# Kernel optimization log

Hardware: AMD Instinct MI355X
Metric: run time of the kernel (lower is better)

Reference implementation:

```python
import jax, jax.numpy as jnp
import numpy as np

B, S, D = 4, 1024, 1024
DH = D // 8  # q/k projection dim


def setup_inputs() -> dict:
    key = jax.random.key(0)
    ks = jax.random.split(key, 16)
    std = 0.02
    inp = {
        "drums": jax.random.normal(ks[0], (B, S, D), jnp.float32),
        "vocals": jax.random.normal(ks[1], (B, S, D), jnp.float32),
        "bass": jax.random.normal(ks[2], (B, S, D), jnp.float32),
        "other": jax.random.normal(ks[3], (B, S, D), jnp.float32),
        # Linear weights stored [in, out] (transposed vs torch's [out, in])
        "DqW": jax.random.normal(ks[4], (D, DH), jnp.float32) * std,
        "Dqb": jax.random.normal(ks[5], (DH,), jnp.float32) * std,
        "DkW": jax.random.normal(ks[6], (D, DH), jnp.float32) * std,
        "Dkb": jax.random.normal(ks[7], (DH,), jnp.float32) * std,
        "DvW": jax.random.normal(ks[8], (D, D), jnp.float32) * std,
        "Dvb": jax.random.normal(ks[9], (D,), jnp.float32) * std,
        "VqW": jax.random.normal(ks[10], (D, DH), jnp.float32) * std,
        "Vqb": jax.random.normal(ks[11], (DH,), jnp.float32) * std,
        "VkW": jax.random.normal(ks[12], (D, DH), jnp.float32) * std,
        "Vkb": jax.random.normal(ks[13], (DH,), jnp.float32) * std,
        "VvW": jax.random.normal(ks[14], (D, D), jnp.float32) * std,
        "Vvb": jax.random.normal(ks[15], (D,), jnp.float32) * std,
    }
    return inp


def reference(drums, vocals, bass, other,
              DqW, Dqb, DkW, Dkb, DvW, Dvb,
              VqW, Vqb, VkW, Vkb, VvW, Vvb):
    d_model = drums.shape[-1]
    lin = lambda x, W, b: jnp.einsum("bsd,de->bse", x, W) + b
    # drums uses D_* projections; vocals/bass/other all use V_* (faithful to source)
    q = jnp.concatenate([lin(drums, DqW, Dqb), lin(vocals, VqW, Vqb),
                         lin(bass, VqW, Vqb), lin(other, VqW, Vqb)], axis=-2)
    k = jnp.concatenate([lin(drums, DkW, Dkb), lin(vocals, VkW, Vkb),
                         lin(bass, VkW, Vkb), lin(other, VkW, Vkb)], axis=-2)
    v = jnp.concatenate([lin(drums, DvW, Dvb), lin(vocals, VvW, Vvb),
                         lin(bass, VvW, Vvb), lin(other, VvW, Vvb)], axis=-2)
    # scores: [B, 4S, 4S]; dropout is identity at inference
    scores = jnp.einsum("bqe,bke->bqk", q, k) / jnp.sqrt(jnp.asarray(d_model, q.dtype))
    attn = jax.nn.softmax(scores, axis=-1)
    out = jnp.einsum("bqk,bkd->bqd", attn, v)  # [B, 4S, D]
    return out.mean(axis=-2)  # [B, D]
```

## Files before the change

### kernel.cpp

```cpp
#include <hip/hip_runtime.h>
#include <hip/hip_bf16.h>

typedef __bf16 bf16x8 __attribute__((ext_vector_type(8)));
typedef float  f32x4  __attribute__((ext_vector_type(4)));

#define MFMA(a, b, c) __builtin_amdgcn_mfma_f32_16x16x32_bf16((a), (b), (c), 0, 0, 0)

static constexpr float SC_L2E = 0.03125f * 1.44269504088896341f;
static constexpr float INV_NQ = 1.0f / 4096.0f;

__device__ inline bf16x8 ld_cvt_bf8(const float* __restrict__ p) {
    f32x4 x0 = *(const f32x4*)p;
    f32x4 x1 = *(const f32x4*)(p + 4);
    bf16x8 r;
    r[0] = (__bf16)x0[0]; r[1] = (__bf16)x0[1]; r[2] = (__bf16)x0[2]; r[3] = (__bf16)x0[3];
    r[4] = (__bf16)x1[0]; r[5] = (__bf16)x1[1]; r[6] = (__bf16)x1[2]; r[7] = (__bf16)x1[3];
    return r;
}

__global__ __launch_bounds__(256) void kT(const float* __restrict__ Dq, const float* __restrict__ Vq,
                                          const float* __restrict__ Dk, const float* __restrict__ Vk,
                                          __bf16* __restrict__ Wt) {
    int idx = blockIdx.x * 256 + threadIdx.x;
    int m   = idx >> 17;
    int rem = idx & 131071;
    int r   = rem >> 7;
    int c   = rem & 127;
    const float* W = (m == 0) ? Dq : (m == 1) ? Vq : (m == 2) ? Dk : Vk;
    Wt[(size_t)m * 131072 + (size_t)c * 1024 + r] = (__bf16)W[rem];
}

__global__ __launch_bounds__(256) void kProj(
    const float* __restrict__ drums, const float* __restrict__ vocals,
    const float* __restrict__ bass,  const float* __restrict__ other,
    const float* __restrict__ Dqb, const float* __restrict__ Vqb,
    const float* __restrict__ Dkb, const float* __restrict__ Vkb,
    const __bf16* __restrict__ Wt, __bf16* __restrict__ Qb, __bf16* __restrict__ Kb) {
    int grow0 = blockIdx.x * 64;
    int b    = grow0 >> 12;
    int r4   = grow0 & 4095;
    int stem = r4 >> 10;
    int rin  = r4 & 1023;

    const float* X = (stem == 0) ? drums : (stem == 1) ? vocals : (stem == 2) ? bass : other;
    const __bf16* WQ = Wt + (size_t)((stem == 0) ? 0 : 1) * 131072;
    const __bf16* WK = Wt + (size_t)((stem == 0) ? 2 : 3) * 131072;
    const float* bQ = (stem == 0) ? Dqb : Vqb;
    const float* bK = (stem == 0) ? Dkb : Vkb;

    int lane = threadIdx.x & 63, wid = threadIdx.x >> 6;
    int l16 = lane & 15, g = lane >> 4;
    int wr = rin + wid * 16;

    f32x4 aQ[8], aK[8];
#pragma unroll
    for (int j = 0; j < 8; j++) { aQ[j] = (f32x4){0.f,0.f,0.f,0.f}; aK[j] = (f32x4){0.f,0.f,0.f,0.f}; }

    const float* xr = X + ((size_t)b * 1024 + wr + l16) * 1024;
    for (int k0 = 0; k0 < 1024; k0 += 32) {
        int ko = k0 + g * 8;
        bf16x8 a = ld_cvt_bf8(xr + ko);
#pragma unroll
        for (int cf = 0; cf < 8; cf++) {
            bf16x8 wq = *(const bf16x8*)(WQ + (size_t)(cf * 16 + l16) * 1024 + ko);
            aQ[cf] = MFMA(a, wq, aQ[cf]);
            bf16x8 wk = *(const bf16x8*)(WK + (size_t)(cf * 16 + l16) * 1024 + ko);
            aK[cf] = MFMA(a, wk, aK[cf]);
        }
    }
    size_t obase = (size_t)b * 4096 + (size_t)stem * 1024;
#pragma unroll
    for (int cf = 0; cf < 8; cf++) {
        int col = cf * 16 + l16;
        float bvq = bQ[col], bvk = bK[col];
#pragma unroll
        for (int r = 0; r < 4; r++) {
            int row = wr + g * 4 + r;
            Qb[(obase + row) * 128 + col] = (__bf16)(aQ[cf][r] + bvq);
            Kb[(obase + row) * 128 + col] = (__bf16)(aK[cf][r] + bvk);
        }
    }
}

__global__ __launch_bounds__(256) void kRowSum(const __bf16* __restrict__ Qb,
                                               const __bf16* __restrict__ Kb,
                                               float* __restrict__ lsum) {
    __shared__ uint4 ktile[1024];
    int bx = blockIdx.x;
    int cc = bx & 7, tile = (bx >> 3) & 31, b = bx >> 8;
    int lane = threadIdx.x & 63, wid = threadIdx.x >> 6;
    int l16 = lane & 15, g = lane >> 4;
    int R  = tile * 128 + wid * 32;
    int C0 = cc * 512;
    const __bf16* Qr = Qb + (size_t)b * 4096 * 128;
    const __bf16* Kr = Kb + (size_t)b * 4096 * 128;

    bf16x8 a[2][4];
#pragma unroll
    for (int rf = 0; rf < 2; rf++)
#pragma unroll
        for (int kf = 0; kf < 4; kf++)
            a[rf][kf] = *(const bf16x8*)(Qr + (size_t)(R + rf * 16 + l16) * 128 + kf * 32 + g * 8);

    int sr = threadIdx.x >> 2, sseg = threadIdx.x & 3;
    char* kbc = (char*)ktile;
    int swm = (sr & 7) << 4;

    uint4 st[4];
    {
        const char* src = (const char*)(Kr + (size_t)(C0 + sr) * 128) + sseg * 64;
#pragma unroll
        for (int j = 0; j < 4; j++) st[j] = *(const uint4*)(src + j * 16);
    }

    float rs[2][4] = {};
    for (int s = 0; s < 8; ++s) {
        __syncthreads();
#pragma unroll
        for (int j = 0; j < 4; j++)
            *(uint4*)(kbc + sr * 256 + ((sseg * 64 + j * 16) ^ swm)) = st[j];
        __syncthreads();
        if (s < 7) {
            const char* src = (const char*)(Kr + (size_t)(C0 + (s + 1) * 64 + sr) * 128) + sseg * 64;
#pragma unroll
            for (int j = 0; j < 4; j++) st[j] = *(const uint4*)(src + j * 16);
        }
#pragma unroll
        for (int ctl = 0; ctl < 4; ++ctl) {
            int r2 = ctl * 16 + l16;
            int rm = (r2 & 7) << 4;
            f32x4 acc0 = (f32x4){0.f,0.f,0.f,0.f};
            f32x4 acc1 = (f32x4){0.f,0.f,0.f,0.f};
#pragma unroll
            for (int kf = 0; kf < 4; kf++) {
                bf16x8 bv = *(const bf16x8*)(kbc + r2 * 256 + ((kf * 64 + g * 16) ^ rm));
                acc0 = MFMA(a[0][kf], bv, acc0);
                acc1 = MFMA(a[1][kf], bv, acc1);
            }
#pragma unroll
            for (int r = 0; r < 4; r++) {
                rs[0][r] += exp2f(acc0[r] * SC_L2E);
                rs[1][r] += exp2f(acc1[r] * SC_L2E);
            }
        }
    }
#pragma unroll
    for (int rf = 0; rf < 2; rf++)
#pragma unroll
        for (int r = 0; r < 4; r++) {
            float v = rs[rf][r];
#pragma unroll
            for (int m = 1; m < 16; m <<= 1) v += __shfl_xor(v, m);
            if (l16 == 0) atomicAdd(&lsum[(size_t)b * 4096 + R + rf * 16 + g * 4 + r], v);
        }
}

__global__ __launch_bounds__(256) void kInv(const float* __restrict__ lsum, float* __restrict__ linv) {
    int i = (blockIdx.x * 256 + threadIdx.x) * 4;
    f32x4 v = *(const f32x4*)(lsum + i);
    f32x4 r = (f32x4){1.f / v[0], 1.f / v[1], 1.f / v[2], 1.f / v[3]};
    *(f32x4*)(linv + i) = r;
}

__global__ __launch_bounds__(256) void kColSum(const __bf16* __restrict__ Qb,
                                               const __bf16* __restrict__ Kb,
                                               const float* __restrict__ linv,
                                               float* __restrict__ wsum) {
    __shared__ uint4 qtile[1024];
    __shared__ float li[512];
    int bx = blockIdx.x;
    int rc = bx & 7, tile = (bx >> 3) & 31, b = bx >> 8;
    int lane = threadIdx.x & 63, wid = threadIdx.x >> 6;
    int l16 = lane & 15, g = lane >> 4;
    int C  = tile * 128 + wid * 32;
    int R0 = rc * 512;
    const __bf16* Qr = Qb + (size_t)b * 4096 * 128;
    const __bf16* Kr = Kb + (size_t)b * 4096 * 128;

    if (threadIdx.x < 128)
        *(f32x4*)(li + threadIdx.x * 4) = *(const f32x4*)(linv + (size_t)b * 4096 + R0 + threadIdx.x * 4);

    bf16x8 kb[2][4];
#pragma unroll
    for (int cf = 0; cf < 2; cf++)
#pragma unroll
        for (int kf = 0; kf < 4; kf++)
            kb[cf][kf] = *(const bf16x8*)(Kr + (size_t)(C + cf * 16 + l16) * 128 + kf * 32 + g * 8);

    int sr = threadIdx.x >> 2, sseg = threadIdx.x & 3;
    char* qbc = (char*)qtile;
    int swm = (sr & 7) << 4;

    uint4 st[4];
    {
        const char* src = (const char*)(Qr + (size_t)(R0 + sr) * 128) + sseg * 64;
#pragma unroll
        for (int j = 0; j < 4; j++) st[j] = *(const uint4*)(src + j * 16);
    }

    float cs[2] = {0.f, 0.f};
    for (int s = 0; s < 8; ++s) {
        __syncthreads();
#pragma unroll
        for (int j = 0; j < 4; j++)
            *(uint4*)(qbc + sr * 256 + ((sseg * 64 + j * 16) ^ swm)) = st[j];
        __syncthreads();
        if (s < 7) {
            const char* src = (const char*)(Qr + (size_t)(R0 + (s + 1) * 64 + sr) * 128) + sseg * 64;
#pragma unroll
            for (int j = 0; j < 4; j++) st[j] = *(const uint4*)(src + j * 16);
        }
#pragma unroll
        for (int ctl = 0; ctl < 4; ++ctl) {
            int r2 = ctl * 16 + l16;
            int rm = (r2 & 7) << 4;
            f32x4 acc0 = (f32x4){0.f,0.f,0.f,0.f};
            f32x4 acc1 = (f32x4){0.f,0.f,0.f,0.f};
#pragma unroll
            for (int kf = 0; kf < 4; kf++) {
                bf16x8 av = *(const bf16x8*)(qbc + r2 * 256 + ((kf * 64 + g * 16) ^ rm));
                acc0 = MFMA(av, kb[0][kf], acc0);
                acc1 = MFMA(av, kb[1][kf], acc1);
            }
            int ib = s * 64 + ctl * 16 + g * 4;
#pragma unroll
            for (int r = 0; r < 4; r++) {
                float lv = li[ib + r];
                cs[0] += exp2f(acc0[r] * SC_L2E) * lv;
                cs[1] += exp2f(acc1[r] * SC_L2E) * lv;
            }
        }
    }
#pragma unroll
    for (int cf = 0; cf < 2; cf++) {
        float v = cs[cf];
        v += __shfl_xor(v, 16);
        v += __shfl_xor(v, 32);
        if (lane < 16) atomicAdd(&wsum[(size_t)b * 4096 + C + cf * 16 + lane], v);
    }
}

__global__ __launch_bounds__(256) void kY(
    const float* __restrict__ drums, const float* __restrict__ vocals,
    const float* __restrict__ bass,  const float* __restrict__ other,
    const float* __restrict__ wsum, float* __restrict__ y, float* __restrict__ alpha) {
    __shared__ float ws[64];
    int bx = blockIdx.x;
    int b = bx >> 6, stem = (bx >> 4) & 3, kc = bx & 15;
    const float* X = (stem == 0) ? drums : (stem == 1) ? vocals : (stem == 2) ? bass : other;
    int t = threadIdx.x;
    if (t < 64) ws[t] = wsum[(size_t)b * 4096 + stem * 1024 + kc * 64 + t] * INV_NQ;
    __syncthreads();

    f32x4 acc = (f32x4){0.f, 0.f, 0.f, 0.f};
    const float* xp = X + ((size_t)b * 1024 + kc * 64) * 1024 + t * 4;
#pragma unroll 4
    for (int i = 0; i < 64; i++) {
        f32x4 xv = *(const f32x4*)(xp + (size_t)i * 1024);
        float wv = ws[i];
        acc[0] += wv * xv[0]; acc[1] += wv * xv[1]; acc[2] += wv * xv[2]; acc[3] += wv * xv[3];
    }
    int seg = (stem == 0) ? 0 : 1;
    float* yp = y + ((size_t)b * 2 + seg) * 1024 + t * 4;
    atomicAdd(yp + 0, acc[0]); atomicAdd(yp + 1, acc[1]);
    atomicAdd(yp + 2, acc[2]); atomicAdd(yp + 3, acc[3]);

    if (t < 64) {
        float s = ws[t];
#pragma unroll
        for (int m = 32; m > 0; m >>= 1) s += __shfl_down(s, m);
        if (t == 0) atomicAdd(alpha + b * 2 + seg, s);
    }
}

__global__ __launch_bounds__(256) void kFinal(
    const float* __restrict__ DvW, const float* __restrict__ Dvb,
    const float* __restrict__ VvW, const float* __restrict__ Vvb,
    const float* __restrict__ y, const float* __restrict__ alpha,
    float* __restrict__ out) {
    __shared__ float yD[128], yV[128];
    int bx = blockIdx.x;
    int b = bx >> 5, dstripe = (bx >> 3) & 3, kc = bx & 7;
    int t = threadIdx.x;
    if (t < 128) {
        yD[t] = y[((size_t)b * 2 + 0) * 1024 + kc * 128 + t];
        yV[t] = y[((size_t)b * 2 + 1) * 1024 + kc * 128 + t];
    }
    __syncthreads();

    int d = dstripe * 256 + t;
    const float* pD = DvW + (size_t)(kc * 128) * 1024 + d;
    const float* pV = VvW + (size_t)(kc * 128) * 1024 + d;
    float acc = 0.f;
#pragma unroll 4
    for (int k = 0; k < 128; k++)
        acc += yD[k] * pD[(size_t)k * 1024] + yV[k] * pV[(size_t)k * 1024];
    if (kc == 0) acc += alpha[b * 2] * Dvb[d] + alpha[b * 2 + 1] * Vvb[d];
    atomicAdd(out + (size_t)b * 1024 + d, acc);
}

extern "C" void kernel_launch(void* const* d_in, const int* in_sizes, int n_in,
                              void* d_out, int out_size, void* d_ws, size_t ws_size,
                              hipStream_t stream) {
    const float* drums  = (const float*)d_in[0];
    const float* vocals = (const float*)d_in[1];
    const float* bass   = (const float*)d_in[2];
    const float* other  = (const float*)d_in[3];
    const float* DqW = (const float*)d_in[4];
    const float* Dqb = (const float*)d_in[5];
    const float* DkW = (const float*)d_in[6];
    const float* Dkb = (const float*)d_in[7];
    const float* DvW = (const float*)d_in[8];
    const float* Dvb = (const float*)d_in[9];
    const float* VqW = (const float*)d_in[10];
    const float* Vqb = (const float*)d_in[11];
    const float* VkW = (const float*)d_in[12];
    const float* Vkb = (const float*)d_in[13];
    const float* VvW = (const float*)d_in[14];
    const float* Vvb = (const float*)d_in[15];
    float* out = (float*)d_out;

    char* ws = (char*)d_ws;
    __bf16* Qb   = (__bf16*)(ws);
    __bf16* Kb   = (__bf16*)(ws + (4u << 20));
    __bf16* Wt   = (__bf16*)(ws + (8u << 20));
    float*  lsum = (float*)(ws + (9u << 20));
    float*  wsum = (float*)(ws + (9u << 20) + (64u << 10));
    float*  y    = (float*)(ws + (9u << 20) + (128u << 10));
    float*  alph = (float*)(ws + (9u << 20) + (160u << 10));
    float*  linv = (float*)(ws + (9u << 20) + (192u << 10));

    hipMemsetAsync(lsum, 0, (160u << 10) + 32, stream);
    hipMemsetAsync(out, 0, (size_t)out_size * sizeof(float), stream);

    kT<<<2048, 256, 0, stream>>>(DqW, VqW, DkW, VkW, Wt);
    kProj<<<256, 256, 0, stream>>>(drums, vocals, bass, other, Dqb, Vqb, Dkb, Vkb, Wt, Qb, Kb);
    kRowSum<<<1024, 256, 0, stream>>>(Qb, Kb, lsum);
    kInv<<<16, 256, 0, stream>>>(lsum, linv);
    kColSum<<<1024, 256, 0, stream>>>(Qb, Kb, linv, wsum);
    kY<<<256, 256, 0, stream>>>(drums, vocals, bass, other, wsum, y, alph);
    kFinal<<<128, 256, 0, stream>>>(DvW, Dvb, VvW, Vvb, y, alph, out);
}
```

Baseline: 329.7 us.

## Raise block counts in projection, reduction kernels and tile weight transpose via LDS

The weight transpose kernel now stages 64x64 tiles in shared memory, so both its reads and its writes are coalesced. The Q/K projection gives each block 16 rows instead of 64 and splits the 128 output columns across its four waves, launching 1024 blocks instead of 256. The kY and kFinal reductions use smaller chunks to raise grid size, at the cost of more atomic adds. The goal is to fill the 256 CUs of the mi355x. The trade-off is that the projection now rereads the input rows once per wave, with less reuse per block.

Measured after the change: 355.5 us. 1.08x slower.

```diff
diff --git a/kernel.cpp b/kernel.cpp
--- a/kernel.cpp
+++ b/kernel.cpp
@@ -21,13 +21,23 @@
 __global__ __launch_bounds__(256) void kT(const float* __restrict__ Dq, const float* __restrict__ Vq,
                                           const float* __restrict__ Dk, const float* __restrict__ Vk,
                                           __bf16* __restrict__ Wt) {
-    int idx = blockIdx.x * 256 + threadIdx.x;
-    int m   = idx >> 17;
-    int rem = idx & 131071;
-    int r   = rem >> 7;
-    int c   = rem & 127;
+    __shared__ float tile[64][65];
+    int bx = blockIdx.x;
+    int m = bx >> 5, rt = (bx >> 1) & 15, ct = bx & 1;
     const float* W = (m == 0) ? Dq : (m == 1) ? Vq : (m == 2) ? Dk : Vk;
-    Wt[(size_t)m * 131072 + (size_t)c * 1024 + r] = (__bf16)W[rem];
+    int t = threadIdx.x;
+    int tr = t >> 6, tc = t & 63;
+#pragma unroll
+    for (int i = 0; i < 16; i++) {
+        int rl = tr + i * 4;
+        tile[rl][tc] = W[(size_t)(rt * 64 + rl) * 128 + ct * 64 + tc];
+    }
+    __syncthreads();
+#pragma unroll
+    for (int i = 0; i < 16; i++) {
+        int cl = tr + i * 4;
+        Wt[(size_t)m * 131072 + (size_t)(ct * 64 + cl) * 1024 + rt * 64 + tc] = (__bf16)tile[tc][cl];
+    }
 }
 
 __global__ __launch_bounds__(256) void kProj(
@@ -36,7 +46,7 @@
     const float* __restrict__ Dqb, const float* __restrict__ Vqb,
     const float* __restrict__ Dkb, const float* __restrict__ Vkb,
     const __bf16* __restrict__ Wt, __bf16* __restrict__ Qb, __bf16* __restrict__ Kb) {
-    int grow0 = blockIdx.x * 64;
+    int grow0 = blockIdx.x * 16;
     int b    = grow0 >> 12;
     int r4   = grow0 & 4095;
     int stem = r4 >> 10;
@@ -50,32 +60,33 @@
 
     int lane = threadIdx.x & 63, wid = threadIdx.x >> 6;
     int l16 = lane & 15, g = lane >> 4;
-    int wr = rin + wid * 16;
-
-    f32x4 aQ[8], aK[8];
-#pragma unroll
-    for (int j = 0; j < 8; j++) { aQ[j] = (f32x4){0.f,0.f,0.f,0.f}; aK[j] = (f32x4){0.f,0.f,0.f,0.f}; }
-
-    const float* xr = X + ((size_t)b * 1024 + wr + l16) * 1024;
+
+    f32x4 aQ[2], aK[2];
+#pragma unroll
+    for (int j = 0; j < 2; j++) { aQ[j] = (f32x4){0.f,0.f,0.f,0.f}; aK[j] = (f32x4){0.f,0.f,0.f,0.f}; }
+
+    const float*  xr  = X  + ((size_t)b * 1024 + rin + l16) * 1024;
+    const __bf16* wq0 = WQ + (size_t)(wid * 32 + l16) * 1024;
+    const __bf16* wq1 = wq0 + 16 * 1024;
+    const __bf16* wk0 = WK + (size_t)(wid * 32 + l16) * 1024;
+    const __bf16* wk1 = wk0 + 16 * 1024;
+
     for (int k0 = 0; k0 < 1024; k0 += 32) {
         int ko = k0 + g * 8;
         bf16x8 a = ld_cvt_bf8(xr + ko);
-#pragma unroll
-        for (int cf = 0; cf < 8; cf++) {
-            bf16x8 wq = *(const bf16x8*)(WQ + (size_t)(cf * 16 + l16) * 1024 + ko);
-            aQ[cf] = MFMA(a, wq, aQ[cf]);
-            bf16x8 wk = *(const bf16x8*)(WK + (size_t)(cf * 16 + l16) * 1024 + ko);
-            aK[cf] = MFMA(a, wk, aK[cf]);
-        }
-    }
-    size_t obase = (size_t)b * 4096 + (size_t)stem * 1024;
-#pragma unroll
-    for (int cf = 0; cf < 8; cf++) {
-        int col = cf * 16 + l16;
+        aQ[0] = MFMA(a, *(const bf16x8*)(wq0 + ko), aQ[0]);
+        aQ[1] = MFMA(a, *(const bf16x8*)(wq1 + ko), aQ[1]);
+        aK[0] = MFMA(a, *(const bf16x8*)(wk0 + ko), aK[0]);
+        aK[1] = MFMA(a, *(const bf16x8*)(wk1 + ko), aK[1]);
+    }
+    size_t obase = (size_t)b * 4096 + (size_t)stem * 1024 + rin;
+#pragma unroll
+    for (int cf = 0; cf < 2; cf++) {
+        int col = (wid * 2 + cf) * 16 + l16;
         float bvq = bQ[col], bvk = bK[col];
 #pragma unroll
         for (int r = 0; r < 4; r++) {
-            int row = wr + g * 4 + r;
+            int row = g * 4 + r;
             Qb[(obase + row) * 128 + col] = (__bf16)(aQ[cf][r] + bvq);
             Kb[(obase + row) * 128 + col] = (__bf16)(aK[cf][r] + bvk);
         }
@@ -244,31 +255,32 @@
     const float* __restrict__ drums, const float* __restrict__ vocals,
     const float* __restrict__ bass,  const float* __restrict__ other,
     const float* __restrict__ wsum, float* __restrict__ y, float* __restrict__ alpha) {
-    __shared__ float ws[64];
-    int bx = blockIdx.x;
-    int b = bx >> 6, stem = (bx >> 4) & 3, kc = bx & 15;
+    __shared__ float ws[16];
+    int bx = blockIdx.x;
+    int b = bx >> 8, stem = (bx >> 6) & 3, kc = bx & 63;
     const float* X = (stem == 0) ? drums : (stem == 1) ? vocals : (stem == 2) ? bass : other;
     int t = threadIdx.x;
-    if (t < 64) ws[t] = wsum[(size_t)b * 4096 + stem * 1024 + kc * 64 + t] * INV_NQ;
+    float wv = 0.f;
+    if (t < 16) { wv = wsum[(size_t)b * 4096 + stem * 1024 + kc * 16 + t] * INV_NQ; ws[t] = wv; }
     __syncthreads();
 
     f32x4 acc = (f32x4){0.f, 0.f, 0.f, 0.f};
-    const float* xp = X + ((size_t)b * 1024 + kc * 64) * 1024 + t * 4;
+    const float* xp = X + ((size_t)b * 1024 + kc * 16) * 1024 + t * 4;
 #pragma unroll 4
-    for (int i = 0; i < 64; i++) {
+    for (int i = 0; i < 16; i++) {
         f32x4 xv = *(const f32x4*)(xp + (size_t)i * 1024);
-        float wv = ws[i];
-        acc[0] += wv * xv[0]; acc[1] += wv * xv[1]; acc[2] += wv * xv[2]; acc[3] += wv * xv[3];
+        float wvi = ws[i];
+        acc[0] += wvi * xv[0]; acc[1] += wvi * xv[1]; acc[2] += wvi * xv[2]; acc[3] += wvi * xv[3];
     }
     int seg = (stem == 0) ? 0 : 1;
     float* yp = y + ((size_t)b * 2 + seg) * 1024 + t * 4;
     atomicAdd(yp + 0, acc[0]); atomicAdd(yp + 1, acc[1]);
     atomicAdd(yp + 2, acc[2]); atomicAdd(yp + 3, acc[3]);
 
-    if (t < 64) {
-        float s = ws[t];
-#pragma unroll
-        for (int m = 32; m > 0; m >>= 1) s += __shfl_down(s, m);
+    if (t < 16) {
+        float s = wv;
+        s += __shfl_xor(s, 1); s += __shfl_xor(s, 2);
+        s += __shfl_xor(s, 4); s += __shfl_xor(s, 8);
         if (t == 0) atomicAdd(alpha + b * 2 + seg, s);
     }
 }
@@ -278,22 +290,22 @@
     const float* __restrict__ VvW, const float* __restrict__ Vvb,
     const float* __restrict__ y, const float* __restrict__ alpha,
     float* __restrict__ out) {
-    __shared__ float yD[128], yV[128];
-    int bx = blockIdx.x;
-    int b = bx >> 5, dstripe = (bx >> 3) & 3, kc = bx & 7;
+    __shared__ float yD[32], yV[32];
+    int bx = blockIdx.x;
+    int b = bx >> 7, dstripe = (bx >> 5) & 3, kc = bx & 31;
     int t = threadIdx.x;
-    if (t < 128) {
-        yD[t] = y[((size_t)b * 2 + 0) * 1024 + kc * 128 + t];
-        yV[t] = y[((size_t)b * 2 + 1) * 1024 + kc * 128 + t];
+    if (t < 32) {
+        yD[t] = y[((size_t)b * 2 + 0) * 1024 + kc * 32 + t];
+        yV[t] = y[((size_t)b * 2 + 1) * 1024 + kc * 32 + t];
     }
     __syncthreads();
 
     int d = dstripe * 256 + t;
-    const float* pD = DvW + (size_t)(kc * 128) * 1024 + d;
-    const float* pV = VvW + (size_t)(kc * 128) * 1024 + d;
+    const float* pD = DvW + (size_t)(kc * 32) * 1024 + d;
+    const float* pV = VvW + (size_t)(kc * 32) * 1024 + d;
     float acc = 0.f;
 #pragma unroll 4
-    for (int k = 0; k < 128; k++)
+    for (int k = 0; k < 32; k++)
         acc += yD[k] * pD[(size_t)k * 1024] + yV[k] * pV[(size_t)k * 1024];
     if (kc == 0) acc += alpha[b * 2] * Dvb[d] + alpha[b * 2 + 1] * Vvb[d];
     atomicAdd(out + (size_t)b * 1024 + d, acc);
@@ -333,11 +345,11 @@
     hipMemsetAsync(lsum, 0, (160u << 10) + 32, stream);
     hipMemsetAsync(out, 0, (size_t)out_size * sizeof(float), stream);
 
-    kT<<<2048, 256, 0, stream>>>(DqW, VqW, DkW, VkW, Wt);
-    kProj<<<256, 256, 0, stream>>>(drums, vocals, bass, other, Dqb, Vqb, Dkb, Vkb, Wt, Qb, Kb);
+    kT<<<128, 256, 0, stream>>>(DqW, VqW, DkW, VkW, Wt);
+    kProj<<<1024, 256, 0, stream>>>(drums, vocals, bass, other, Dqb, Vqb, Dkb, Vkb, Wt, Qb, Kb);
     kRowSum<<<1024, 256, 0, stream>>>(Qb, Kb, lsum);
     kInv<<<16, 256, 0, stream>>>(lsum, linv);
     kColSum<<<1024, 256, 0, stream>>>(Qb, Kb, linv, wsum);
-    kY<<<256, 256, 0, stream>>>(drums, vocals, bass, other, wsum, y, alph);
-    kFinal<<<128, 256, 0, stream>>>(DvW, Dvb, VvW, Vvb, y, alph, out);
-}
+    kY<<<1024, 256, 0, stream>>>(drums, vocals, bass, other, wsum, y, alph);
+    kFinal<<<512, 256, 0, stream>>>(DvW, Dvb, VvW, Vvb, y, alph, out);
+}
```
